# Kernel tuning notes

Hardware: AMD Instinct MI355X
Metric: run time of the kernel (lower is better)

Reference implementation:

```python
import jax, jax.numpy as jnp
import numpy as np
import math

B, S, D_IN = 128, 1024, 1024
NQ, NB, NH = 8, 256, 4  # num_qubits (embed dim), bottleneck_dim, attention heads


def _mha(x, w_in, b_in, w_out, b_out, num_heads):
    # Faithful torch nn.MultiheadAttention (batch_first=False): x is [L, N, E]
    L, N, E = x.shape
    Dh = E // num_heads
    qkv = x @ w_in.T + b_in                      # [L, N, 3E]
    q, k, v = jnp.split(qkv, 3, axis=-1)
    q = q.reshape(L, N, num_heads, Dh)
    k = k.reshape(L, N, num_heads, Dh)
    v = v.reshape(L, N, num_heads, Dh)
    scores = jnp.einsum('lnhd,mnhd->nhlm', q, k) / jnp.sqrt(jnp.asarray(Dh, x.dtype))
    attn = jax.nn.softmax(scores, axis=-1)       # softmax over keys (dim m)
    o = jnp.einsum('nhlm,mnhd->lnhd', attn, v).reshape(L, N, E)
    return o @ w_out.T + b_out


def setup_inputs() -> dict:
    key = jax.random.key(0)
    ks = jax.random.split(key, 12)
    s_in = 1.0 / np.sqrt(D_IN)
    s_q = 1.0 / np.sqrt(NQ)
    s_b = 1.0 / np.sqrt(NB)
    return {
        'x': jax.random.normal(ks[0], (B, S, D_IN), jnp.float32),
        'amp_w': jax.random.uniform(ks[1], (NQ, D_IN), jnp.float32, -s_in, s_in),
        'amp_b': jax.random.uniform(ks[2], (NQ,), jnp.float32, -s_in, s_in),
        'phase_w': jax.random.uniform(ks[3], (NQ, D_IN), jnp.float32, -s_in, s_in),
        'phase_b': jax.random.uniform(ks[4], (NQ,), jnp.float32, -s_in, s_in),
        'in_proj_w': jax.random.uniform(ks[5], (3 * NQ, NQ), jnp.float32, -s_q, s_q),
        'in_proj_b': jnp.zeros((3 * NQ,), jnp.float32),
        'out_proj_w': jax.random.uniform(ks[6], (NQ, NQ), jnp.float32, -s_q, s_q),
        'out_proj_b': jnp.zeros((NQ,), jnp.float32),
        'meas_w': jax.random.uniform(ks[7], (NB, NQ), jnp.float32, -s_q, s_q),
        'meas_b': jax.random.uniform(ks[8], (NB,), jnp.float32, -s_q, s_q),
        'unc_w': jax.random.uniform(ks[9], (NB, NB), jnp.float32, -s_b, s_b),
        'unc_b': jax.random.uniform(ks[10], (NB,), jnp.float32, -s_b, s_b),
    }


def reference(x, amp_w, amp_b, phase_w, phase_b, in_proj_w, in_proj_b,
              out_proj_w, out_proj_b, meas_w, meas_b, unc_w, unc_b):
    two_pi = jnp.asarray(2.0 * math.pi, x.dtype)
    amplitudes = jnp.tanh(x @ amp_w.T + amp_b)                   # [B, S, NQ]
    phases = jax.nn.sigmoid(x @ phase_w.T + phase_b) * two_pi    # [B, S, NQ]
    # quantum_states = amplitudes * exp(i*phases); take real/imag parts
    real_part = amplitudes * jnp.cos(phases)
    imag_part = amplitudes * jnp.sin(phases)
    # torch MHA with batch_first=False treats dim0 (B) as seq length L, dim1 (S) as batch N
    ent_real = _mha(real_part, in_proj_w, in_proj_b, out_proj_w, out_proj_b, NH)
    ent_imag = _mha(imag_part, in_proj_w, in_proj_b, out_proj_w, out_proj_b, NH)
    measured = jnp.sqrt(ent_real ** 2 + ent_imag ** 2)
    compressed = measured @ meas_w.T + meas_b                    # [B, S, NB]
    uncertainty = jax.nn.sigmoid(compressed @ unc_w.T + unc_b)
    return (compressed, uncertainty)
```

## Files before the change

### kernel.cpp

```cpp
#include <hip/hip_runtime.h>
#include <math.h>

#define B_   128
#define S_   1024
#define DIN  1024
#define NQ_  8
#define NB_  256
#define ROWS (B_ * S_)

__global__ __launch_bounds__(256) void k0_compose(
    const float* __restrict__ meas_w, const float* __restrict__ meas_b,
    const float* __restrict__ unc_w, const float* __restrict__ unc_b,
    float* __restrict__ W2, float* __restrict__ b2) {
  int i = threadIdx.x;
  float acc[NQ_] = {0.f, 0.f, 0.f, 0.f, 0.f, 0.f, 0.f, 0.f};
  float accb = 0.f;
  for (int k = 0; k < NB_; ++k) {
    float u = unc_w[i * NB_ + k];
#pragma unroll
    for (int j = 0; j < NQ_; ++j) acc[j] += u * meas_w[k * NQ_ + j];
    accb += u * meas_b[k];
  }
#pragma unroll
  for (int j = 0; j < NQ_; ++j) W2[i * NQ_ + j] = acc[j];
  b2[i] = unc_b[i] + accb;
}

__global__ __launch_bounds__(256) void k1_proj(
    const float* __restrict__ x,
    const float* __restrict__ amp_w, const float* __restrict__ amp_b,
    const float* __restrict__ phase_w, const float* __restrict__ phase_b,
    float* __restrict__ rp, float* __restrict__ ip) {
  int row = blockIdx.x * blockDim.x + threadIdx.x;
  const float4* xr = (const float4*)(x + (size_t)row * DIN);
  float acc[16];
#pragma unroll
  for (int j = 0; j < 16; ++j) acc[j] = 0.f;

  for (int k4 = 0; k4 < DIN / 4; ++k4) {
    float4 xv = xr[k4];
#pragma unroll
    for (int kk = 0; kk < 4; ++kk) {
      int k = k4 * 4 + kk;
      float xk = (kk == 0) ? xv.x : (kk == 1) ? xv.y : (kk == 2) ? xv.z : xv.w;
#pragma unroll
      for (int j = 0; j < 8; ++j) {
        acc[j]     += xk * amp_w[j * DIN + k];
        acc[8 + j] += xk * phase_w[j * DIN + k];
      }
    }
  }

  float out_r[8], out_i[8];
  const float two_pi = 6.28318530717958647692f;
#pragma unroll
  for (int j = 0; j < 8; ++j) {
    float a  = tanhf(acc[j] + amp_b[j]);
    float ph = two_pi / (1.f + expf(-(acc[8 + j] + phase_b[j])));
    float s, c;
    sincosf(ph, &s, &c);
    out_r[j] = a * c;
    out_i[j] = a * s;
  }
  float4* rp4 = (float4*)(rp + (size_t)row * NQ_);
  float4* ip4 = (float4*)(ip + (size_t)row * NQ_);
  rp4[0] = make_float4(out_r[0], out_r[1], out_r[2], out_r[3]);
  rp4[1] = make_float4(out_r[4], out_r[5], out_r[6], out_r[7]);
  ip4[0] = make_float4(out_i[0], out_i[1], out_i[2], out_i[3]);
  ip4[1] = make_float4(out_i[4], out_i[5], out_i[6], out_i[7]);
}

__global__ __launch_bounds__(128) void k2_attn(
    const float* __restrict__ rp, const float* __restrict__ ip,
    const float* __restrict__ in_w, const float* __restrict__ in_b,
    const float* __restrict__ out_w, const float* __restrict__ out_b,
    float* __restrict__ measured) {
  int n = blockIdx.x;
  int tid = threadIdx.x;

  __shared__ float q_lds[2][128][9];
  __shared__ float kv_lds[2][128][17];
  __shared__ float o_lds[2][128][9];

  {
    int l = tid;
#pragma unroll
    for (int p = 0; p < 2; ++p) {
      const float* src = (p == 0 ? rp : ip) + (size_t)l * (S_ * NQ_) + (size_t)n * NQ_;
      float xv[8];
#pragma unroll
      for (int j = 0; j < 8; ++j) xv[j] = src[j];
#pragma unroll
      for (int c = 0; c < 24; ++c) {
        float acc = in_b[c];
#pragma unroll
        for (int j = 0; j < 8; ++j) acc += in_w[c * 8 + j] * xv[j];
        if (c < 8) q_lds[p][l][c] = acc;
        else       kv_lds[p][l][c - 8] = acc;
      }
    }
  }
  __syncthreads();

  {
    int p = tid >> 6, h = (tid >> 4) & 3, lb = tid & 15;
    float q0[8], q1[8], o0[8], o1[8], ssum[8];
#pragma unroll
    for (int r = 0; r < 8; ++r) {
      q0[r] = q_lds[p][lb * 8 + r][2 * h];
      q1[r] = q_lds[p][lb * 8 + r][2 * h + 1];
      o0[r] = 0.f; o1[r] = 0.f; ssum[r] = 0.f;
    }
    const float scale = 0.70710678118654752440f;
    for (int m = 0; m < 128; ++m) {
      float k0 = kv_lds[p][m][2 * h];
      float k1 = kv_lds[p][m][2 * h + 1];
      float v0 = kv_lds[p][m][8 + 2 * h];
      float v1 = kv_lds[p][m][8 + 2 * h + 1];
#pragma unroll
      for (int r = 0; r < 8; ++r) {
        float s = (q0[r] * k0 + q1[r] * k1) * scale;
        float e = expf(s);
        ssum[r] += e;
        o0[r] += e * v0;
        o1[r] += e * v1;
      }
    }
#pragma unroll
    for (int r = 0; r < 8; ++r) {
      float inv = 1.f / ssum[r];
      o_lds[p][lb * 8 + r][2 * h]     = o0[r] * inv;
      o_lds[p][lb * 8 + r][2 * h + 1] = o1[r] * inv;
    }
  }
  __syncthreads();

  {
    int l = tid;
    float res[2][8];
#pragma unroll
    for (int p = 0; p < 2; ++p) {
      float ov[8];
#pragma unroll
      for (int c = 0; c < 8; ++c) ov[c] = o_lds[p][l][c];
#pragma unroll
      for (int j = 0; j < 8; ++j) {
        float acc = out_b[j];
#pragma unroll
        for (int c = 0; c < 8; ++c) acc += out_w[j * 8 + c] * ov[c];
        res[p][j] = acc;
      }
    }
    float* dst = measured + (size_t)l * (S_ * NQ_) + (size_t)n * NQ_;
#pragma unroll
    for (int j = 0; j < 8; ++j)
      dst[j] = sqrtf(res[0][j] * res[0][j] + res[1][j] * res[1][j]);
  }
}

__global__ __launch_bounds__(256) void k3_out(
    const float* __restrict__ measured,
    const float* __restrict__ meas_w, const float* __restrict__ meas_b,
    const float* __restrict__ W2, const float* __restrict__ b2,
    float* __restrict__ out_c, float* __restrict__ out_u) {
  int i = threadIdx.x;
  float w1[8], w2[8];
#pragma unroll
  for (int j = 0; j < 8; ++j) {
    w1[j] = meas_w[i * 8 + j];
    w2[j] = W2[i * 8 + j];
  }
  float b1 = meas_b[i], bu = b2[i];
  int r0 = blockIdx.x * 64;
  for (int rr = 0; rr < 64; ++rr) {
    int r = r0 + rr;
    const float* m = measured + (size_t)r * NQ_;
    float mv[8];
#pragma unroll
    for (int j = 0; j < 8; ++j) mv[j] = m[j];
    float c = b1, u = bu;
#pragma unroll
    for (int j = 0; j < 8; ++j) {
      c += w1[j] * mv[j];
      u += w2[j] * mv[j];
    }
    out_c[(size_t)r * NB_ + i] = c;
    out_u[(size_t)r * NB_ + i] = 1.f / (1.f + expf(-u));
  }
}

extern "C" void kernel_launch(void* const* d_in, const int* in_sizes, int n_in,
                              void* d_out, int out_size, void* d_ws, size_t ws_size,
                              hipStream_t stream) {
  (void)in_sizes; (void)n_in; (void)out_size; (void)ws_size;
  const float* x       = (const float*)d_in[0];
  const float* amp_w   = (const float*)d_in[1];
  const float* amp_b   = (const float*)d_in[2];
  const float* phase_w = (const float*)d_in[3];
  const float* phase_b = (const float*)d_in[4];
  const float* in_w    = (const float*)d_in[5];
  const float* in_b    = (const float*)d_in[6];
  const float* out_w   = (const float*)d_in[7];
  const float* out_b   = (const float*)d_in[8];
  const float* meas_w  = (const float*)d_in[9];
  const float* meas_b  = (const float*)d_in[10];
  const float* unc_w   = (const float*)d_in[11];
  const float* unc_b   = (const float*)d_in[12];

  float* ws       = (float*)d_ws;
  float* rp       = ws;
  float* ip       = rp + 1048576;
  float* measured = ip + 1048576;
  float* W2       = measured + 1048576;
  float* b2       = W2 + 2048;
  float* out_c    = (float*)d_out;
  float* out_u    = out_c + (size_t)ROWS * NB_;

  hipLaunchKernelGGL(k0_compose, dim3(1), dim3(256), 0, stream,
                     meas_w, meas_b, unc_w, unc_b, W2, b2);
  hipLaunchKernelGGL(k1_proj, dim3(ROWS / 256), dim3(256), 0, stream,
                     x, amp_w, amp_b, phase_w, phase_b, rp, ip);
  hipLaunchKernelGGL(k2_attn, dim3(S_), dim3(128), 0, stream,
                     rp, ip, in_w, in_b, out_w, out_b, measured);
  hipLaunchKernelGGL(k3_out, dim3(ROWS / 64), dim3(256), 0, stream,
                     measured, meas_w, meas_b, W2, b2, out_c, out_u);
}
```

Baseline: 986.8 us.

## Stage x tiles through swizzled LDS with coalesced loads and transpose intermediates

k1_proj used to have each thread read its own 4KB row of x, which gives fully uncoalesced global loads. It now loads 256x32 tiles cooperatively into XOR-swizzled shared memory and prefetches the next tile into registers. The projection weights are pre-transposed into an interleaved [k][16] layout so each k step reads contiguous, wave-uniform weights. The rp/ip/measured intermediates are stored in [S][B] order, so k2_attn reads and writes contiguously and k3_out pays for the strided reads instead. The cost is extra shared memory, more registers for the staging buffers, and two barriers per K step.

```diff
diff --git a/kernel.cpp b/kernel.cpp
--- a/kernel.cpp
+++ b/kernel.cpp
@@ -7,11 +7,13 @@
 #define NQ_  8
 #define NB_  256
 #define ROWS (B_ * S_)
+#define KT   32
 
 __global__ __launch_bounds__(256) void k0_compose(
     const float* __restrict__ meas_w, const float* __restrict__ meas_b,
     const float* __restrict__ unc_w, const float* __restrict__ unc_b,
-    float* __restrict__ W2, float* __restrict__ b2) {
+    const float* __restrict__ amp_w, const float* __restrict__ phase_w,
+    float* __restrict__ W2, float* __restrict__ b2, float* __restrict__ wq) {
   int i = threadIdx.x;
   float acc[NQ_] = {0.f, 0.f, 0.f, 0.f, 0.f, 0.f, 0.f, 0.f};
   float accb = 0.f;
@@ -24,31 +26,70 @@
 #pragma unroll
   for (int j = 0; j < NQ_; ++j) W2[i * NQ_ + j] = acc[j];
   b2[i] = unc_b[i] + accb;
+
+#pragma unroll
+  for (int kk = 0; kk < 4; ++kk) {
+    int k = i * 4 + kk;
+#pragma unroll
+    for (int j = 0; j < NQ_; ++j) {
+      wq[k * 16 + j]     = amp_w[j * DIN + k];
+      wq[k * 16 + 8 + j] = phase_w[j * DIN + k];
+    }
+  }
 }
 
 __global__ __launch_bounds__(256) void k1_proj(
-    const float* __restrict__ x,
-    const float* __restrict__ amp_w, const float* __restrict__ amp_b,
-    const float* __restrict__ phase_w, const float* __restrict__ phase_b,
-    float* __restrict__ rp, float* __restrict__ ip) {
-  int row = blockIdx.x * blockDim.x + threadIdx.x;
-  const float4* xr = (const float4*)(x + (size_t)row * DIN);
+    const float* __restrict__ x, const float* __restrict__ wq,
+    const float* __restrict__ amp_b, const float* __restrict__ phase_b,
+    float* __restrict__ rp_t, float* __restrict__ ip_t) {
+  int tid = threadIdx.x;
+  int row0 = blockIdx.x * 256;
+
+  __shared__ float4 tile[256][8];
+
+  int lr = tid >> 3;
+  int lc = tid & 7;
+  int pc = lc ^ (lr & 7);
+  int sw = tid & 7;
+
   float acc[16];
 #pragma unroll
   for (int j = 0; j < 16; ++j) acc[j] = 0.f;
 
-  for (int k4 = 0; k4 < DIN / 4; ++k4) {
-    float4 xv = xr[k4];
-#pragma unroll
-    for (int kk = 0; kk < 4; ++kk) {
-      int k = k4 * 4 + kk;
-      float xk = (kk == 0) ? xv.x : (kk == 1) ? xv.y : (kk == 2) ? xv.z : xv.w;
-#pragma unroll
-      for (int j = 0; j < 8; ++j) {
-        acc[j]     += xk * amp_w[j * DIN + k];
-        acc[8 + j] += xk * phase_w[j * DIN + k];
-      }
-    }
+  const float* xb = x + (size_t)row0 * DIN;
+  float4 stg[8];
+#pragma unroll
+  for (int i = 0; i < 8; ++i)
+    stg[i] = *(const float4*)(xb + (size_t)(lr + i * 32) * DIN + lc * 4);
+
+  for (int step = 0; step < DIN / KT; ++step) {
+#pragma unroll
+    for (int i = 0; i < 8; ++i) tile[lr + i * 32][pc] = stg[i];
+    __syncthreads();
+
+    if (step + 1 < DIN / KT) {
+      const float* xs = xb + (step + 1) * KT;
+#pragma unroll
+      for (int i = 0; i < 8; ++i)
+        stg[i] = *(const float4*)(xs + (size_t)(lr + i * 32) * DIN + lc * 4);
+    }
+
+    const float* wk = wq + step * KT * 16;
+#pragma unroll
+    for (int c4 = 0; c4 < 8; ++c4) {
+      float4 xv = tile[tid][c4 ^ sw];
+#pragma unroll
+      for (int kk = 0; kk < 4; ++kk) {
+        float xk = (kk == 0) ? xv.x : (kk == 1) ? xv.y : (kk == 2) ? xv.z : xv.w;
+        const float* w = wk + (c4 * 4 + kk) * 16;
+#pragma unroll
+        for (int j = 0; j < 8; ++j) {
+          acc[j]     += xk * w[j];
+          acc[8 + j] += xk * w[8 + j];
+        }
+      }
+    }
+    __syncthreads();
   }
 
   float out_r[8], out_i[8];
@@ -62,8 +103,10 @@
     out_r[j] = a * c;
     out_i[j] = a * s;
   }
-  float4* rp4 = (float4*)(rp + (size_t)row * NQ_);
-  float4* ip4 = (float4*)(ip + (size_t)row * NQ_);
+  int row = row0 + tid;
+  size_t toff = ((size_t)(row & (S_ - 1)) * B_ + (size_t)(row >> 10)) * NQ_;
+  float4* rp4 = (float4*)(rp_t + toff);
+  float4* ip4 = (float4*)(ip_t + toff);
   rp4[0] = make_float4(out_r[0], out_r[1], out_r[2], out_r[3]);
   rp4[1] = make_float4(out_r[4], out_r[5], out_r[6], out_r[7]);
   ip4[0] = make_float4(out_i[0], out_i[1], out_i[2], out_i[3]);
@@ -71,10 +114,10 @@
 }
 
 __global__ __launch_bounds__(128) void k2_attn(
-    const float* __restrict__ rp, const float* __restrict__ ip,
+    const float* __restrict__ rp_t, const float* __restrict__ ip_t,
     const float* __restrict__ in_w, const float* __restrict__ in_b,
     const float* __restrict__ out_w, const float* __restrict__ out_b,
-    float* __restrict__ measured) {
+    float* __restrict__ measured_t) {
   int n = blockIdx.x;
   int tid = threadIdx.x;
 
@@ -86,7 +129,7 @@
     int l = tid;
 #pragma unroll
     for (int p = 0; p < 2; ++p) {
-      const float* src = (p == 0 ? rp : ip) + (size_t)l * (S_ * NQ_) + (size_t)n * NQ_;
+      const float* src = (p == 0 ? rp_t : ip_t) + ((size_t)n * B_ + l) * NQ_;
       float xv[8];
 #pragma unroll
       for (int j = 0; j < 8; ++j) xv[j] = src[j];
@@ -151,7 +194,7 @@
         res[p][j] = acc;
       }
     }
-    float* dst = measured + (size_t)l * (S_ * NQ_) + (size_t)n * NQ_;
+    float* dst = measured_t + ((size_t)n * B_ + l) * NQ_;
 #pragma unroll
     for (int j = 0; j < 8; ++j)
       dst[j] = sqrtf(res[0][j] * res[0][j] + res[1][j] * res[1][j]);
@@ -159,7 +202,7 @@
 }
 
 __global__ __launch_bounds__(256) void k3_out(
-    const float* __restrict__ measured,
+    const float* __restrict__ measured_t,
     const float* __restrict__ meas_w, const float* __restrict__ meas_b,
     const float* __restrict__ W2, const float* __restrict__ b2,
     float* __restrict__ out_c, float* __restrict__ out_u) {
@@ -174,7 +217,8 @@
   int r0 = blockIdx.x * 64;
   for (int rr = 0; rr < 64; ++rr) {
     int r = r0 + rr;
-    const float* m = measured + (size_t)r * NQ_;
+    const float* m = measured_t +
+        ((size_t)(r & (S_ - 1)) * B_ + (size_t)(r >> 10)) * NQ_;
     float mv[8];
 #pragma unroll
     for (int j = 0; j < 8; ++j) mv[j] = m[j];
@@ -207,21 +251,22 @@
   const float* unc_w   = (const float*)d_in[11];
   const float* unc_b   = (const float*)d_in[12];
 
-  float* ws       = (float*)d_ws;
-  float* rp       = ws;
-  float* ip       = rp + 1048576;
-  float* measured = ip + 1048576;
-  float* W2       = measured + 1048576;
-  float* b2       = W2 + 2048;
-  float* out_c    = (float*)d_out;
-  float* out_u    = out_c + (size_t)ROWS * NB_;
+  float* ws         = (float*)d_ws;
+  float* rp_t       = ws;
+  float* ip_t       = rp_t + 1048576;
+  float* measured_t = ip_t + 1048576;
+  float* W2         = measured_t + 1048576;
+  float* b2         = W2 + 2048;
+  float* wq         = b2 + 256;
+  float* out_c      = (float*)d_out;
+  float* out_u      = out_c + (size_t)ROWS * NB_;
 
   hipLaunchKernelGGL(k0_compose, dim3(1), dim3(256), 0, stream,
-                     meas_w, meas_b, unc_w, unc_b, W2, b2);
+                     meas_w, meas_b, unc_w, unc_b, amp_w, phase_w, W2, b2, wq);
   hipLaunchKernelGGL(k1_proj, dim3(ROWS / 256), dim3(256), 0, stream,
-                     x, amp_w, amp_b, phase_w, phase_b, rp, ip);
+                     x, wq, amp_b, phase_b, rp_t, ip_t);
   hipLaunchKernelGGL(k2_attn, dim3(S_), dim3(128), 0, stream,
-                     rp, ip, in_w, in_b, out_w, out_b, measured);
+                     rp_t, ip_t, in_w, in_b, out_w, out_b, measured_t);
   hipLaunchKernelGGL(k3_out, dim3(ROWS / 64), dim3(256), 0, stream,
-                     measured, meas_w, meas_b, W2, b2, out_c, out_u);
-}
+                     measured_t, meas_w, meas_b, W2, b2, out_c, out_u);
+}
```

Result: slower. 1.072 ms (+8.6%).
